# Kernel optimization log

Measured on AMD Instinct MI355X. Metric: run time of the kernel, lower is better.

The kernel has to match this reference:

```python
import jax, jax.numpy as jnp
import numpy as np
from jax import lax

B, T, IN, H = 4096, 512, 11, 16


def lstm(x, Wih, Whh, bih, bhh):
    # x: [B, T, in]; PyTorch gate order i, f, g, o packed along 4H.
    xg = jnp.einsum('bti,gi->btg', x, Wih) + bih + bhh  # [B, T, 4H]
    h0 = jnp.zeros((x.shape[0], Whh.shape[1]), x.dtype)
    c0 = jnp.zeros_like(h0)

    def step(carry, xg_t):
        h, c = carry
        g = xg_t + h @ Whh.T                      # [B, 4H]
        i, f, gg, o = jnp.split(g, 4, axis=-1)
        i = jax.nn.sigmoid(i)
        f = jax.nn.sigmoid(f)
        gg = jnp.tanh(gg)
        o = jax.nn.sigmoid(o)
        c = f * c + i * gg
        h = o * jnp.tanh(c)
        return (h, c), h

    _, hs = lax.scan(step, (h0, c0), jnp.swapaxes(xg, 0, 1))  # hs: [T, B, H]
    return jnp.swapaxes(hs, 0, 1)  # [B, T, H]


def setup_inputs() -> dict:
    key = jax.random.key(0)
    ks = jax.random.split(key, 16)
    s = 1.0 / np.sqrt(H)
    u = lambda k, shape: jax.random.uniform(k, shape, jnp.float32, -s, s)
    return {
        'x': jax.random.normal(ks[0], (B, T, IN), jnp.float32),
        'Wih1': u(ks[1], (4 * H, IN)), 'Whh1': u(ks[2], (4 * H, H)),
        'bih1': u(ks[3], (4 * H,)), 'bhh1': u(ks[4], (4 * H,)),
        'Wih2': u(ks[5], (4 * H, H)), 'Whh2': u(ks[6], (4 * H, H)),
        'bih2': u(ks[7], (4 * H,)), 'bhh2': u(ks[8], (4 * H,)),
        'Wd1': u(ks[9], (8, H)), 'bd1': u(ks[10], (8,)),
        'Wd2': u(ks[11], (8, 8)), 'bd2': u(ks[12], (8,)),
        'Wd3': u(ks[13], (3, 8)), 'bd3': u(ks[14], (3,)),
    }


def reference(x, Wih1, Whh1, bih1, bhh1, Wih2, Whh2, bih2, bhh2,
              Wd1, bd1, Wd2, bd2, Wd3, bd3):
    h1 = lstm(x, Wih1, Whh1, bih1, bhh1)          # [B, T, H]
    # Dropout2d treated as identity (eval mode).
    h2 = lstm(h1, Wih2, Whh2, bih2, bhh2)          # [B, T, H]
    s = jax.nn.softmax(h2, axis=1)[:, -1, :]       # softmax over TIME, take last step -> [B, H]
    d = (s @ Wd1.T + bd1) @ Wd2.T + bd2
    d = d @ Wd3.T + bd3                            # [B, 3]
    return jax.nn.softmax(d, axis=1)
```

## Files before the change

kernel.cpp:

```cpp
#include <hip/hip_runtime.h>

#define T_STEPS 512
#define IN_DIM 11
#define ROW_PAD 12
#define H_DIM 16
#define ROW_F (T_STEPS * IN_DIM)
#define CHUNK_T 16
#define CHUNK_F (CHUNK_T * IN_DIM)
#define N_CHUNK (T_STEPS / CHUNK_T)
#define LOG2E 1.44269504088896340736f

typedef _Float16 v2h __attribute__((ext_vector_type(2)));
typedef _Float16 v8h __attribute__((ext_vector_type(8)));

#if __has_builtin(__builtin_amdgcn_fdot2)
__device__ __forceinline__ float fdot2(v2h a, v2h b, float c) {
    return __builtin_amdgcn_fdot2(a, b, c, false);
}
#else
__device__ __forceinline__ float fdot2(v2h a, v2h b, float c) {
    float d;
    asm("v_dot2_f32_f16 %0, %1, %2, %3" : "=v"(d) : "v"(a), "v"(b), "v"(c));
    return d;
}
#endif

template<int CTRL>
__device__ __forceinline__ float qperm(float v) {
    return __builtin_bit_cast(float,
        __builtin_amdgcn_update_dpp(0, __builtin_bit_cast(int, v),
                                    CTRL, 0xf, 0xf, true));
}

__device__ __forceinline__ float bcast_lane(float v, int l) {
    return __builtin_bit_cast(float,
        __builtin_amdgcn_readlane(__builtin_bit_cast(int, v), l));
}

__global__ __launch_bounds__(256)
__attribute__((amdgpu_waves_per_eu(4, 4)))
void lstm2_head(
    const float* __restrict__ x,
    const float* __restrict__ Wih1, const float* __restrict__ Whh1,
    const float* __restrict__ bih1, const float* __restrict__ bhh1,
    const float* __restrict__ Wih2, const float* __restrict__ Whh2,
    const float* __restrict__ bih2, const float* __restrict__ bhh2,
    const float* __restrict__ Wd1, const float* __restrict__ bd1,
    const float* __restrict__ Wd2, const float* __restrict__ bd2,
    const float* __restrict__ Wd3, const float* __restrict__ bd3,
    float* __restrict__ out)
{
    __shared__ _Float16 xlds[4][2][216];
    __shared__ v8h      shh8[4][2][2];

    const int lane = threadIdx.x & 63;
    const int wid = __builtin_amdgcn_readfirstlane((int)(threadIdx.x >> 6));
    const int b = blockIdx.x * 4 + wid;

    const int r   = lane >> 2;
    const int gt  = lane & 3;
    const int row = gt * H_DIM + r;

    const bool is_t = (gt == 2);
    const float M   = is_t ? (-2.0f * LOG2E) : (-LOG2E);
    const float vAa = is_t ? 2.0f : 1.0f;
    const float vBc = is_t ? -1.0f : 0.0f;

    v2h wi1h[6], wh1h[8], wi2h[8], wh2h[8];
    #pragma unroll
    for (int j = 0; j < 5; ++j)
        wi1h[j] = (v2h){(_Float16)(M * Wih1[row * IN_DIM + 2 * j]),
                        (_Float16)(M * Wih1[row * IN_DIM + 2 * j + 1])};
    wi1h[5] = (v2h){(_Float16)(M * Wih1[row * IN_DIM + 10]), (_Float16)0.0f};
    #pragma unroll
    for (int j = 0; j < 8; ++j) {
        wh1h[j] = (v2h){(_Float16)(M * Whh1[row * H_DIM + 2 * j]),
                        (_Float16)(M * Whh1[row * H_DIM + 2 * j + 1])};
        wi2h[j] = (v2h){(_Float16)(M * Wih2[row * H_DIM + 2 * j]),
                        (_Float16)(M * Wih2[row * H_DIM + 2 * j + 1])};
        wh2h[j] = (v2h){(_Float16)(M * Whh2[row * H_DIM + 2 * j]),
                        (_Float16)(M * Whh2[row * H_DIM + 2 * j + 1])};
    }
    const float bb1 = M * (bih1[row] + bhh1[row]);
    const float bb2 = M * (bih2[row] + bhh2[row]);
    #pragma unroll
    for (int j = 0; j < 6; ++j) asm volatile("" : "+v"(wi1h[j]));
    #pragma unroll
    for (int j = 0; j < 8; ++j) {
        asm volatile("" : "+v"(wh1h[j]));
        asm volatile("" : "+v"(wi2h[j]));
        asm volatile("" : "+v"(wh2h[j]));
    }

    const float* __restrict__ xb = x + (size_t)b * ROW_F;
    _Float16* const xl0 = &xlds[wid][0][0];
    _Float16* const xl1 = &xlds[wid][1][0];
    _Float16* const h1w = (_Float16*)&shh8[wid][0][0];
    _Float16* const h2w = (_Float16*)&shh8[wid][1][0];

    h1w[r] = (_Float16)0.0f;
    h2w[r] = (_Float16)0.0f;
    if (lane < 32) {
        const int buf = lane >> 4, rr = lane & 15;
        xlds[wid][buf][rr * ROW_PAD + IN_DIM] = (_Float16)0.0f;
    }

    const int f1i = lane, f2i = lane + 64, f3i = lane + 128;
    const int p1 = (f1i / IN_DIM) * ROW_PAD + (f1i % IN_DIM);
    const int p2 = (f2i / IN_DIM) * ROW_PAD + (f2i % IN_DIM);
    const int p3 = (f3i / IN_DIM) * ROW_PAD + (f3i % IN_DIM);

    float gl0 = xb[f1i];
    float gl1 = xb[f2i];
    float gl2 = xb[min(f3i, ROW_F - 1)];

    float c1 = 0.f, c2 = 0.f, h2v = 0.f, ssum = 0.f;
    v2h h1r[8], h2r[8];
    #pragma unroll
    for (int j = 0; j < 8; ++j) {
        h1r[j] = (v2h){(_Float16)0.f, (_Float16)0.f};
        h2r[j] = (v2h){(_Float16)0.f, (_Float16)0.f};
    }

    for (int ck = 0; ck < N_CHUNK; ++ck) {
        _Float16* const xbuf = (ck & 1) ? xl1 : xl0;
        xbuf[p1] = (_Float16)gl0;
        xbuf[p2] = (_Float16)gl1;
        xbuf[p3] = (_Float16)gl2;
        if (ck + 1 < N_CHUNK) {
            const int base = (ck + 1) * CHUNK_F;
            gl0 = xb[base + f1i];
            gl1 = xb[base + f2i];
            gl2 = xb[min(base + f3i, ROW_F - 1)];
        }

        #pragma unroll
        for (int t2 = 0; t2 < CHUNK_T; ++t2) {
            const v2h* const xr = (const v2h*)(xbuf + t2 * ROW_PAD);

            float a2 = bb2, b2 = 0.f;
            #pragma unroll
            for (int j = 0; j < 4; ++j) {
                a2 = fdot2(wh2h[j],     h2r[j],     a2);
                b2 = fdot2(wh2h[j + 4], h2r[j + 4], b2);
            }

            float a1 = bb1, b1 = 0.f;
            #pragma unroll
            for (int j = 0; j < 3; ++j) {
                a1 = fdot2(wi1h[j],     xr[j],     a1);
                b1 = fdot2(wi1h[j + 3], xr[j + 3], b1);
            }
            #pragma unroll
            for (int j = 0; j < 4; ++j) {
                a1 = fdot2(wh1h[j],     h1r[j],     a1);
                b1 = fdot2(wh1h[j + 4], h1r[j + 4], b1);
            }

            const float g1 = a1 + b1;
            const float act1 = __builtin_fmaf(vAa,
                __builtin_amdgcn_rcpf(1.0f + __builtin_amdgcn_exp2f(g1)), vBc);
            {
                const float gi = qperm<0x00>(act1);
                const float gf = qperm<0x55>(act1);
                const float gg = qperm<0xAA>(act1);
                const float go = qperm<0xFF>(act1);
                c1 = __builtin_fmaf(gf, c1, gi * gg);
                const float tc = __builtin_fmaf(2.0f,
                    __builtin_amdgcn_rcpf(1.0f +
                        __builtin_amdgcn_exp2f(-2.0f * LOG2E * c1)), -1.0f);
                h1w[r] = (_Float16)(go * tc);
            }
            {
                const v2h* hp = (const v2h*)h1w;
                #pragma unroll
                for (int j = 0; j < 8; ++j) h1r[j] = hp[j];
            }
            #pragma unroll
            for (int j = 0; j < 4; ++j) {
                a2 = fdot2(wi2h[j],     h1r[j],     a2);
                b2 = fdot2(wi2h[j + 4], h1r[j + 4], b2);
            }

            const float g2 = a2 + b2;
            const float act2 = __builtin_fmaf(vAa,
                __builtin_amdgcn_rcpf(1.0f + __builtin_amdgcn_exp2f(g2)), vBc);
            {
                const float gi = qperm<0x00>(act2);
                const float gf = qperm<0x55>(act2);
                const float gg = qperm<0xAA>(act2);
                const float go = qperm<0xFF>(act2);
                c2 = __builtin_fmaf(gf, c2, gi * gg);
                const float tc = __builtin_fmaf(2.0f,
                    __builtin_amdgcn_rcpf(1.0f +
                        __builtin_amdgcn_exp2f(-2.0f * LOG2E * c2)), -1.0f);
                h2v = go * tc;
                h2w[r] = (_Float16)h2v;
            }
            {
                const v2h* hp = (const v2h*)h2w;
                #pragma unroll
                for (int j = 0; j < 8; ++j) h2r[j] = hp[j];
            }

            ssum += __builtin_amdgcn_exp2f(LOG2E * h2v);
        }
    }

    const float sv = __builtin_amdgcn_exp2f(LOG2E * h2v) / ssum;

    float ssb[H_DIM];
    #pragma unroll
    for (int k = 0; k < H_DIM; ++k) ssb[k] = bcast_lane(sv, 4 * k);

    const int r8 = lane & 7;
    float acc1 = bd1[r8];
    #pragma unroll
    for (int k = 0; k < H_DIM; ++k)
        acc1 = __builtin_fmaf(Wd1[r8 * H_DIM + k], ssb[k], acc1);

    float d1s[8];
    #pragma unroll
    for (int j = 0; j < 8; ++j) d1s[j] = bcast_lane(acc1, j);

    float acc2 = bd2[r8];
    #pragma unroll
    for (int k = 0; k < 8; ++k)
        acc2 = __builtin_fmaf(Wd2[r8 * 8 + k], d1s[k], acc2);

    float d2s[8];
    #pragma unroll
    for (int j = 0; j < 8; ++j) d2s[j] = bcast_lane(acc2, j);

    float lg = 0.f;
    if (lane < 3) {
        lg = bd3[lane];
        #pragma unroll
        for (int k = 0; k < 8; ++k)
            lg = __builtin_fmaf(Wd3[lane * 8 + k], d2s[k], lg);
    }
    const float l0 = bcast_lane(lg, 0);
    const float l1 = bcast_lane(lg, 1);
    const float l2 = bcast_lane(lg, 2);
    const float mx = fmaxf(l0, fmaxf(l1, l2));
    const float e0 = __builtin_amdgcn_exp2f(LOG2E * (l0 - mx));
    const float e1 = __builtin_amdgcn_exp2f(LOG2E * (l1 - mx));
    const float e2 = __builtin_amdgcn_exp2f(LOG2E * (l2 - mx));
    const float inv = 1.0f / (e0 + e1 + e2);
    if (lane < 3) {
        const float ev = (lane == 0) ? e0 : ((lane == 1) ? e1 : e2);
        out[b * 3 + lane] = ev * inv;
    }
}

extern "C" void kernel_launch(void* const* d_in, const int* in_sizes, int n_in,
                              void* d_out, int out_size, void* d_ws, size_t ws_size,
                              hipStream_t stream) {
    (void)in_sizes; (void)n_in; (void)out_size; (void)d_ws; (void)ws_size;
    const float* x    = (const float*)d_in[0];
    const float* Wih1 = (const float*)d_in[1];
    const float* Whh1 = (const float*)d_in[2];
    const float* bih1 = (const float*)d_in[3];
    const float* bhh1 = (const float*)d_in[4];
    const float* Wih2 = (const float*)d_in[5];
    const float* Whh2 = (const float*)d_in[6];
    const float* bih2 = (const float*)d_in[7];
    const float* bhh2 = (const float*)d_in[8];
    const float* Wd1  = (const float*)d_in[9];
    const float* bd1  = (const float*)d_in[10];
    const float* Wd2  = (const float*)d_in[11];
    const float* bd2  = (const float*)d_in[12];
    const float* Wd3  = (const float*)d_in[13];
    const float* bd3  = (const float*)d_in[14];

    lstm2_head<<<dim3(4096 / 4), dim3(256), 0, stream>>>(
        x, Wih1, Whh1, bih1, bhh1, Wih2, Whh2, bih2, bhh2,
        Wd1, bd1, Wd2, bd2, Wd3, bd3, (float*)d_out);
}
```

Measured before the change: 455.3 us.

## Precompute layer-1 input projection in a separate kernel, fold tanh scaling into activation

New measurement: 624.9 us. 37.3% more time.

```diff
diff --git a/kernel.cpp b/kernel.cpp
--- a/kernel.cpp
+++ b/kernel.cpp
@@ -4,26 +4,21 @@
 #define IN_DIM 11
 #define ROW_PAD 12
 #define H_DIM 16
+#define G_DIM 64
 #define ROW_F (T_STEPS * IN_DIM)
 #define CHUNK_T 16
 #define CHUNK_F (CHUNK_T * IN_DIM)
 #define N_CHUNK (T_STEPS / CHUNK_T)
 #define LOG2E 1.44269504088896340736f
+#define XG_BYTES ((size_t)4096 * T_STEPS * G_DIM * 2)
 
 typedef _Float16 v2h __attribute__((ext_vector_type(2)));
+typedef _Float16 v4h __attribute__((ext_vector_type(4)));
 typedef _Float16 v8h __attribute__((ext_vector_type(8)));
 
-#if __has_builtin(__builtin_amdgcn_fdot2)
 __device__ __forceinline__ float fdot2(v2h a, v2h b, float c) {
     return __builtin_amdgcn_fdot2(a, b, c, false);
 }
-#else
-__device__ __forceinline__ float fdot2(v2h a, v2h b, float c) {
-    float d;
-    asm("v_dot2_f32_f16 %0, %1, %2, %3" : "=v"(d) : "v"(a), "v"(b), "v"(c));
-    return d;
-}
-#endif
 
 template<int CTRL>
 __device__ __forceinline__ float qperm(float v) {
@@ -37,10 +32,46 @@
         __builtin_amdgcn_readlane(__builtin_bit_cast(int, v), l));
 }
 
+__device__ __forceinline__ v2h pair_lo(v8h v, int) { return (v2h){v[0], v[1]}; }
+
+__global__ __launch_bounds__(256) void xg_pre(
+    const float* __restrict__ x,
+    const float* __restrict__ Wih1,
+    const float* __restrict__ bih1, const float* __restrict__ bhh1,
+    _Float16* __restrict__ xg)
+{
+    const int lane = threadIdx.x & 63;
+    const int wid = __builtin_amdgcn_readfirstlane((int)(threadIdx.x >> 6));
+    const int b = blockIdx.x;
+
+    const int r   = lane >> 2;
+    const int gt  = lane & 3;
+    const int row = gt * H_DIM + r;
+    const float M = (gt == 2) ? (-2.0f * LOG2E) : (-LOG2E);
+
+    float wi[IN_DIM];
+    #pragma unroll
+    for (int k = 0; k < IN_DIM; ++k) wi[k] = M * Wih1[row * IN_DIM + k];
+    const float binit = M * (bih1[row] + bhh1[row]);
+
+    const float* __restrict__ xb = x + (size_t)b * ROW_F;
+    _Float16* __restrict__ og = xg + ((size_t)b * T_STEPS) * G_DIM;
+
+    for (int t = wid * 128; t < wid * 128 + 128; ++t) {
+        const float* __restrict__ xr = xb + t * IN_DIM;
+        float acc = binit;
+        #pragma unroll
+        for (int k = 0; k < IN_DIM; ++k)
+            acc = __builtin_fmaf(wi[k], xr[k], acc);
+        og[(size_t)t * G_DIM + lane] = (_Float16)acc;
+    }
+}
+
+template<bool XG>
 __global__ __launch_bounds__(256)
 __attribute__((amdgpu_waves_per_eu(4, 4)))
 void lstm2_head(
-    const float* __restrict__ x,
+    const float* __restrict__ x, const _Float16* __restrict__ xg,
     const float* __restrict__ Wih1, const float* __restrict__ Whh1,
     const float* __restrict__ bih1, const float* __restrict__ bhh1,
     const float* __restrict__ Wih2, const float* __restrict__ Whh2,
@@ -50,8 +81,8 @@
     const float* __restrict__ Wd3, const float* __restrict__ bd3,
     float* __restrict__ out)
 {
-    __shared__ _Float16 xlds[4][2][216];
-    __shared__ v8h      shh8[4][2][2];
+    __shared__ __align__(16) _Float16 xlds[4][2][XG ? 1024 : 216];
+    __shared__ __align__(16) _Float16 hsl[4][2][16];
 
     const int lane = threadIdx.x & 63;
     const int wid = __builtin_amdgcn_readfirstlane((int)(threadIdx.x >> 6));
@@ -63,15 +94,19 @@
 
     const bool is_t = (gt == 2);
     const float M   = is_t ? (-2.0f * LOG2E) : (-LOG2E);
-    const float vAa = is_t ? 2.0f : 1.0f;
-    const float vBc = is_t ? -1.0f : 0.0f;
+    const float vAa = is_t ? (-4.0f * LOG2E) : 1.0f;
+    const float vBc = is_t ? (2.0f * LOG2E) : 0.0f;
 
     v2h wi1h[6], wh1h[8], wi2h[8], wh2h[8];
-    #pragma unroll
-    for (int j = 0; j < 5; ++j)
-        wi1h[j] = (v2h){(_Float16)(M * Wih1[row * IN_DIM + 2 * j]),
-                        (_Float16)(M * Wih1[row * IN_DIM + 2 * j + 1])};
-    wi1h[5] = (v2h){(_Float16)(M * Wih1[row * IN_DIM + 10]), (_Float16)0.0f};
+    if (!XG) {
+        #pragma unroll
+        for (int j = 0; j < 5; ++j)
+            wi1h[j] = (v2h){(_Float16)(M * Wih1[row * IN_DIM + 2 * j]),
+                            (_Float16)(M * Wih1[row * IN_DIM + 2 * j + 1])};
+        wi1h[5] = (v2h){(_Float16)(M * Wih1[row * IN_DIM + 10]), (_Float16)0.0f};
+        #pragma unroll
+        for (int j = 0; j < 6; ++j) asm volatile("" : "+v"(wi1h[j]));
+    }
     #pragma unroll
     for (int j = 0; j < 8; ++j) {
         wh1h[j] = (v2h){(_Float16)(M * Whh1[row * H_DIM + 2 * j]),
@@ -81,10 +116,8 @@
         wh2h[j] = (v2h){(_Float16)(M * Whh2[row * H_DIM + 2 * j]),
                         (_Float16)(M * Whh2[row * H_DIM + 2 * j + 1])};
     }
-    const float bb1 = M * (bih1[row] + bhh1[row]);
+    const float bb1 = XG ? 0.0f : (M * (bih1[row] + bhh1[row]));
     const float bb2 = M * (bih2[row] + bhh2[row]);
-    #pragma unroll
-    for (int j = 0; j < 6; ++j) asm volatile("" : "+v"(wi1h[j]));
     #pragma unroll
     for (int j = 0; j < 8; ++j) {
         asm volatile("" : "+v"(wh1h[j]));
@@ -92,70 +125,91 @@
         asm volatile("" : "+v"(wh2h[j]));
     }
 
-    const float* __restrict__ xb = x + (size_t)b * ROW_F;
     _Float16* const xl0 = &xlds[wid][0][0];
     _Float16* const xl1 = &xlds[wid][1][0];
-    _Float16* const h1w = (_Float16*)&shh8[wid][0][0];
-    _Float16* const h2w = (_Float16*)&shh8[wid][1][0];
-
-    h1w[r] = (_Float16)0.0f;
-    h2w[r] = (_Float16)0.0f;
-    if (lane < 32) {
-        const int buf = lane >> 4, rr = lane & 15;
-        xlds[wid][buf][rr * ROW_PAD + IN_DIM] = (_Float16)0.0f;
-    }
-
-    const int f1i = lane, f2i = lane + 64, f3i = lane + 128;
-    const int p1 = (f1i / IN_DIM) * ROW_PAD + (f1i % IN_DIM);
-    const int p2 = (f2i / IN_DIM) * ROW_PAD + (f2i % IN_DIM);
-    const int p3 = (f3i / IN_DIM) * ROW_PAD + (f3i % IN_DIM);
-
-    float gl0 = xb[f1i];
-    float gl1 = xb[f2i];
-    float gl2 = xb[min(f3i, ROW_F - 1)];
+    _Float16* const h1w = &hsl[wid][0][0];
+    _Float16* const h2w = &hsl[wid][1][0];
+
+    if (lane < 32) hsl[wid][lane >> 4][lane & 15] = (_Float16)0.0f;
+
+    const float* __restrict__ xb = x + (size_t)b * ROW_F;
+    const uint4* __restrict__ gb4 =
+        (const uint4*)(xg + ((size_t)b * T_STEPS) * G_DIM);
+    int p1 = 0, p2 = 0, p3 = 0;
+    float gl0 = 0.f, gl1 = 0.f, gl2 = 0.f;
+    uint4 ga = {}, gb = {};
+    if (XG) {
+        ga = gb4[lane];
+        gb = gb4[64 + lane];
+    } else {
+        if (lane < 32) {
+            const int buf = lane >> 4, rr = lane & 15;
+            xlds[wid][buf][rr * ROW_PAD + IN_DIM] = (_Float16)0.0f;
+        }
+        const int f1i = lane, f2i = lane + 64, f3i = lane + 128;
+        p1 = (f1i / IN_DIM) * ROW_PAD + (f1i % IN_DIM);
+        p2 = (f2i / IN_DIM) * ROW_PAD + (f2i % IN_DIM);
+        p3 = (f3i / IN_DIM) * ROW_PAD + (f3i % IN_DIM);
+        gl0 = xb[f1i]; gl1 = xb[f2i]; gl2 = xb[min(f3i, ROW_F - 1)];
+    }
 
     float c1 = 0.f, c2 = 0.f, h2v = 0.f, ssum = 0.f;
-    v2h h1r[8], h2r[8];
-    #pragma unroll
-    for (int j = 0; j < 8; ++j) {
-        h1r[j] = (v2h){(_Float16)0.f, (_Float16)0.f};
-        h2r[j] = (v2h){(_Float16)0.f, (_Float16)0.f};
-    }
+    v8h h1a = {}, h1b = {}, h2a = {}, h2b = {};
+
+    #define DOT8(ACC1, ACC2, W, HA, HB)                                        \
+        {                                                                      \
+            ACC1 = fdot2(W[0], (v2h){HA[0], HA[1]}, ACC1);                     \
+            ACC2 = fdot2(W[4], (v2h){HB[0], HB[1]}, ACC2);                     \
+            ACC1 = fdot2(W[1], (v2h){HA[2], HA[3]}, ACC1);                     \
+            ACC2 = fdot2(W[5], (v2h){HB[2], HB[3]}, ACC2);                     \
+            ACC1 = fdot2(W[2], (v2h){HA[4], HA[5]}, ACC1);                     \
+            ACC2 = fdot2(W[6], (v2h){HB[4], HB[5]}, ACC2);                     \
+            ACC1 = fdot2(W[3], (v2h){HA[6], HA[7]}, ACC1);                     \
+            ACC2 = fdot2(W[7], (v2h){HB[6], HB[7]}, ACC2);                     \
+        }
 
     for (int ck = 0; ck < N_CHUNK; ++ck) {
         _Float16* const xbuf = (ck & 1) ? xl1 : xl0;
-        xbuf[p1] = (_Float16)gl0;
-        xbuf[p2] = (_Float16)gl1;
-        xbuf[p3] = (_Float16)gl2;
-        if (ck + 1 < N_CHUNK) {
-            const int base = (ck + 1) * CHUNK_F;
-            gl0 = xb[base + f1i];
-            gl1 = xb[base + f2i];
-            gl2 = xb[min(base + f3i, ROW_F - 1)];
+        if (XG) {
+            ((uint4*)xbuf)[lane]      = ga;
+            ((uint4*)xbuf)[64 + lane] = gb;
+            if (ck + 1 < N_CHUNK) {
+                const uint4* np = gb4 + (size_t)(ck + 1) * 128;
+                ga = np[lane];
+                gb = np[64 + lane];
+            }
+        } else {
+            xbuf[p1] = (_Float16)gl0;
+            xbuf[p2] = (_Float16)gl1;
+            xbuf[p3] = (_Float16)gl2;
+            if (ck + 1 < N_CHUNK) {
+                const int base = (ck + 1) * CHUNK_F;
+                gl0 = xb[base + lane];
+                gl1 = xb[base + lane + 64];
+                gl2 = xb[min(base + lane + 128, ROW_F - 1)];
+            }
         }
 
         #pragma unroll
         for (int t2 = 0; t2 < CHUNK_T; ++t2) {
-            const v2h* const xr = (const v2h*)(xbuf + t2 * ROW_PAD);
-
             float a2 = bb2, b2 = 0.f;
-            #pragma unroll
-            for (int j = 0; j < 4; ++j) {
-                a2 = fdot2(wh2h[j],     h2r[j],     a2);
-                b2 = fdot2(wh2h[j + 4], h2r[j + 4], b2);
-            }
-
-            float a1 = bb1, b1 = 0.f;
-            #pragma unroll
-            for (int j = 0; j < 3; ++j) {
-                a1 = fdot2(wi1h[j],     xr[j],     a1);
-                b1 = fdot2(wi1h[j + 3], xr[j + 3], b1);
-            }
-            #pragma unroll
-            for (int j = 0; j < 4; ++j) {
-                a1 = fdot2(wh1h[j],     h1r[j],     a1);
-                b1 = fdot2(wh1h[j + 4], h1r[j + 4], b1);
-            }
+            DOT8(a2, b2, wh2h, h2a, h2b)
+
+            float a1, b1 = 0.f;
+            if (XG) {
+                a1 = (float)xbuf[t2 * G_DIM + lane];
+            } else {
+                const v4h* xr4 = (const v4h*)(xbuf + t2 * ROW_PAD);
+                const v4h x0 = xr4[0], x1 = xr4[1], x2 = xr4[2];
+                a1 = bb1;
+                a1 = fdot2(wi1h[0], (v2h){x0[0], x0[1]}, a1);
+                b1 = fdot2(wi1h[1], (v2h){x0[2], x0[3]}, b1);
+                a1 = fdot2(wi1h[2], (v2h){x1[0], x1[1]}, a1);
+                b1 = fdot2(wi1h[3], (v2h){x1[2], x1[3]}, b1);
+                a1 = fdot2(wi1h[4], (v2h){x2[0], x2[1]}, a1);
+                b1 = fdot2(wi1h[5], (v2h){x2[2], x2[3]}, b1);
+            }
+            DOT8(a1, b1, wh1h, h1a, h1b)
 
             const float g1 = a1 + b1;
             const float act1 = __builtin_fmaf(vAa,
@@ -167,20 +221,16 @@
                 const float go = qperm<0xFF>(act1);
                 c1 = __builtin_fmaf(gf, c1, gi * gg);
                 const float tc = __builtin_fmaf(2.0f,
-                    __builtin_amdgcn_rcpf(1.0f +
-                        __builtin_amdgcn_exp2f(-2.0f * LOG2E * c1)), -1.0f);
+                    __builtin_amdgcn_rcpf(1.0f + __builtin_amdgcn_exp2f(c1)),
+                    -1.0f);
                 h1w[r] = (_Float16)(go * tc);
             }
-            {
-                const v2h* hp = (const v2h*)h1w;
-                #pragma unroll
-                for (int j = 0; j < 8; ++j) h1r[j] = hp[j];
-            }
-            #pragma unroll
-            for (int j = 0; j < 4; ++j) {
-                a2 = fdot2(wi2h[j],     h1r[j],     a2);
-                b2 = fdot2(wi2h[j + 4], h1r[j + 4], b2);
-            }
+            h1a = ((const v8h*)h1w)[0];
+            h1b = ((const v8h*)h1w)[1];
+
+            float xa2 = 0.f;
+            DOT8(a2, xa2, wi2h, h1a, h1b)
+            b2 += xa2;
 
             const float g2 = a2 + b2;
             const float act2 = __builtin_fmaf(vAa,
@@ -192,20 +242,18 @@
                 const float go = qperm<0xFF>(act2);
                 c2 = __builtin_fmaf(gf, c2, gi * gg);
                 const float tc = __builtin_fmaf(2.0f,
-                    __builtin_amdgcn_rcpf(1.0f +
-                        __builtin_amdgcn_exp2f(-2.0f * LOG2E * c2)), -1.0f);
+                    __builtin_amdgcn_rcpf(1.0f + __builtin_amdgcn_exp2f(c2)),
+                    -1.0f);
                 h2v = go * tc;
                 h2w[r] = (_Float16)h2v;
             }
-            {
-                const v2h* hp = (const v2h*)h2w;
-                #pragma unroll
-                for (int j = 0; j < 8; ++j) h2r[j] = hp[j];
-            }
+            h2a = ((const v8h*)h2w)[0];
+            h2b = ((const v8h*)h2w)[1];
 
             ssum += __builtin_amdgcn_exp2f(LOG2E * h2v);
         }
     }
+    #undef DOT8
 
     const float sv = __builtin_amdgcn_exp2f(LOG2E * h2v) / ssum;
 
@@ -256,7 +304,7 @@
 extern "C" void kernel_launch(void* const* d_in, const int* in_sizes, int n_in,
                               void* d_out, int out_size, void* d_ws, size_t ws_size,
                               hipStream_t stream) {
-    (void)in_sizes; (void)n_in; (void)out_size; (void)d_ws; (void)ws_size;
+    (void)in_sizes; (void)n_in; (void)out_size;
     const float* x    = (const float*)d_in[0];
     const float* Wih1 = (const float*)d_in[1];
     const float* Whh1 = (const float*)d_in[2];
@@ -273,7 +321,16 @@
     const float* Wd3  = (const float*)d_in[13];
     const float* bd3  = (const float*)d_in[14];
 
-    lstm2_head<<<dim3(4096 / 4), dim3(256), 0, stream>>>(
-        x, Wih1, Whh1, bih1, bhh1, Wih2, Whh2, bih2, bhh2,
-        Wd1, bd1, Wd2, bd2, Wd3, bd3, (float*)d_out);
-}
+    if (ws_size >= XG_BYTES) {
+        _Float16* xg = (_Float16*)d_ws;
+        xg_pre<<<dim3(4096), dim3(256), 0, stream>>>(x, Wih1, bih1, bhh1, xg);
+        lstm2_head<true><<<dim3(4096 / 4), dim3(256), 0, stream>>>(
+            x, xg, Wih1, Whh1, bih1, bhh1, Wih2, Whh2, bih2, bhh2,
+            Wd1, bd1, Wd2, bd2, Wd3, bd3, (float*)d_out);
+    } else {
+        lstm2_head<false><<<dim3(4096 / 4), dim3(256), 0, stream>>>(
+            x, (const _Float16*)nullptr, Wih1, Whh1, bih1, bhh1,
+            Wih2, Whh2, bih2, bhh2,
+            Wd1, bd1, Wd2, bd2, Wd3, bd3, (float*)d_out);
+    }
+}
```
